# Performance work log

Hardware: AMD Instinct MI355X
Metric: run time of the kernel (lower is better)

The kernel has to match this reference:

```python
import math
import jax, jax.numpy as jnp
import numpy as np

B, N, DIM, E, G, TOPK, DEPTH = 64, 512, 128, 16, 32, 4, 1
HID = 4 * DIM
EPS = 1e-8
LAMBDA_INIT = 0.8 - 0.6 * math.exp(-0.3 * DEPTH)


def setup_inputs() -> dict:
    key = jax.random.key(0)
    ks = jax.random.split(key, 16)
    d = {}
    d["x"] = jax.random.normal(ks[0], (B, N, DIM), jnp.float32)
    d["bias"] = jnp.zeros((1,), jnp.float32)
    d["attn_scale"] = jnp.ones((DIM,), jnp.float32)
    d["ffn_scale"] = jnp.ones((DIM,), jnp.float32)
    d["Wr"] = jax.random.normal(ks[1], (DIM, E), jnp.float32) * 0.05
    d["br"] = jnp.zeros((E,), jnp.float32)
    d["E1"] = jax.random.uniform(ks[2], (2, E, N, G), jnp.float32)
    d["E2"] = jax.random.uniform(ks[3], (2, E, G, N), jnp.float32)
    d["lambda_q1"] = jax.random.normal(ks[4], (DIM,), jnp.float32) * 0.1
    d["lambda_k1"] = jax.random.normal(ks[5], (DIM,), jnp.float32) * 0.1
    d["lambda_q2"] = jax.random.normal(ks[6], (DIM,), jnp.float32) * 0.1
    d["lambda_k2"] = jax.random.normal(ks[7], (DIM,), jnp.float32) * 0.1
    d["outer_lambda"] = jnp.log(jnp.asarray(99.0, jnp.float32))
    d["W1"] = jax.random.normal(ks[8], (DIM, HID), jnp.float32) * 0.02
    d["b1"] = jnp.zeros((HID,), jnp.float32)
    d["W2"] = jax.random.normal(ks[9], (DIM, HID), jnp.float32) * 0.02
    d["b2"] = jnp.zeros((HID,), jnp.float32)
    d["W3"] = jax.random.normal(ks[10], (HID, DIM), jnp.float32) * 0.02
    d["b3"] = jnp.zeros((DIM,), jnp.float32)
    return d


def _rmsnorm(v, scale):
    # RMSNorm with p<0: full L2 norm over last dim, rms = ||v|| / sqrt(d)
    rms = jnp.linalg.norm(v, axis=-1, keepdims=True) * (DIM ** -0.5)
    return scale * (v / (rms + EPS))


def reference(x, bias, attn_scale, ffn_scale, Wr, br, E1, E2,
              lambda_q1, lambda_k1, lambda_q2, lambda_k2, outer_lambda,
              W1, b1, W2, b2, W3, b3):
    # ---- pre-norm ----
    xn = _rmsnorm(x, attn_scale)                       # [B,N,F]

    # ---- top-k routing (selector) ----
    route_logits = xn @ Wr + br                        # [B,N,E]
    gate = jax.nn.sigmoid(route_logits)
    _, topk_idx = jax.lax.top_k(gate + bias, TOPK)     # [B,N,K]
    mask = jnp.sum(jax.nn.one_hot(topk_idx, E, dtype=gate.dtype), axis=-2)  # [B,N,E]
    # sigmoid(route + log(mask)) == sigmoid(route) * mask (mask in {0,1})
    gated = gate * mask
    route = gated / jnp.sum(gated, axis=-1, keepdims=True)

    # ---- coefficient: concat([1], -(exp(q1.k1) - exp(q2.k2) + lambda_init)) ----
    l1 = jnp.exp(jnp.sum(lambda_q1 * lambda_k1))
    l2 = jnp.exp(jnp.sum(lambda_q2 * lambda_k2))
    lambda_full = -(l1 - l2 + LAMBDA_INIT)
    coef = jnp.concatenate([jnp.ones((1,), x.dtype), lambda_full[None]])  # [2]

    # ---- outer mixing matrix (convex comb of eye with itself -> eye, kept faithful) ----
    w = jax.nn.sigmoid(outer_lambda)
    eye = jnp.eye(DIM, dtype=x.dtype)
    outer = w * eye + (1.0 - w) * eye                  # [F,F]

    # ---- expert graph mixing: bik,e,ekid,ekdj,bjf,fc->bic ----
    A1 = jax.nn.softmax(E1, axis=-1)                   # [2,E,N,G]
    A2 = jax.nn.softmax(E2, axis=-1)                   # [2,E,G,N]
    M = jnp.einsum('ekid,ekdj->ekij', A1, A2)          # [2,E,N,N]
    s = jnp.einsum('bik,ekij->beij', route, M)         # [B,2,N,N]
    xc = jnp.einsum('bjf,fc->bjc', xn, outer)          # [B,N,F]
    attn = jnp.einsum('e,beij,bjc->bic', coef, s, xc)  # [B,N,F]

    x = x + attn

    # ---- SwiGLU FFN (dropout is identity at inference) ----
    xn2 = _rmsnorm(x, ffn_scale)
    h = jax.nn.silu(xn2 @ W1 + b1) * (xn2 @ W2 + b2)   # [B,N,4F]
    x = x + h @ W3 + b3
    return x, topk_idx
```

## Files before the change

### kernel.cpp

```cpp
#include <hip/hip_runtime.h>
#include <math.h>

#define B_ 64
#define N_ 512
#define DIM_ 128
#define E_ 16
#define G_ 32
#define TOPK_ 4
#define HID_ 512

constexpr int BN_ROWS = B_ * N_;

using bf16x8 = __attribute__((ext_vector_type(8))) short;
using s16x4  = __attribute__((ext_vector_type(4))) short;
using f32x4  = __attribute__((ext_vector_type(4))) float;

__device__ __forceinline__ float bf2f(short s) {
    union { unsigned u; float f; } x;
    x.u = ((unsigned)(unsigned short)s) << 16;
    return x.f;
}
__device__ __forceinline__ short f2bf(float f) {
    union { float f; unsigned u; } x;
    x.f = f;
    unsigned r = x.u + 0x7FFF + ((x.u >> 16) & 1);
    return (short)(r >> 16);
}

__device__ __forceinline__ bf16x8 frag_ld(const short* base, int row, int ks, int lhi) {
    int addr = row * 128 + (((ks * 64) + lhi * 16) ^ ((row & 7) << 4));
    return *(const bf16x8*)((const char*)base + addr);
}

constexpr int NPRE = BN_ROWS / 4;
constexpr int NXNT = B_ * 16;
constexpr int NSMG = 32 * 512 / 8;
constexpr int NSMN = 1024 / 4;
constexpr int NTW  = 64 * 3;
constexpr int NMISC = NPRE + NXNT + NSMG + NSMN + NTW + 1;

__global__ __launch_bounds__(256) void k_misc(
    const float* __restrict__ x, const float* __restrict__ attn_s,
    const float* __restrict__ Wr, const float* __restrict__ br, const float* __restrict__ bias,
    float* __restrict__ route, float* __restrict__ topk_out,
    short* __restrict__ xnT,
    const float* __restrict__ E1, short* __restrict__ A1nb,
    const float* __restrict__ E2, short* __restrict__ A2nb,
    const float* __restrict__ W1, const float* __restrict__ W2, const float* __restrict__ W3,
    short* __restrict__ W1T, short* __restrict__ W2T, short* __restrict__ W3T,
    const float* __restrict__ lq1, const float* __restrict__ lk1,
    const float* __restrict__ lq2, const float* __restrict__ lk2,
    float lam_init, float* __restrict__ lam_out) {
    __shared__ float xbuf[4][132];
    __shared__ float tb[32][129];
    __shared__ float invb[32];
    __shared__ float tw[32][33];
    int blk = blockIdx.x;
    int tid = threadIdx.x;

    if (blk < NPRE) {
        int w = tid >> 6, lane = tid & 63;
        int row = blk * 4 + w;
        float2 v = ((const float2*)(x + (size_t)row * DIM_))[lane];
        float ss = v.x * v.x + v.y * v.y;
        for (int off = 32; off; off >>= 1) ss += __shfl_xor(ss, off);
        float inv = 1.0f / (sqrtf(ss * (1.0f / DIM_)) + 1e-8f);
        float2 s = ((const float2*)attn_s)[lane];
        xbuf[w][lane * 2]     = v.x * inv * s.x;
        xbuf[w][lane * 2 + 1] = v.y * inv * s.y;
        int e = lane & 15, chunk = lane >> 4;
        float acc = 0.f;
#pragma unroll
        for (int j = 0; j < 32; ++j) {
            int d = chunk * 32 + j;
            acc += xbuf[w][d] * Wr[d * E_ + e];
        }
        acc += __shfl_xor(acc, 16);
        acc += __shfl_xor(acc, 32);
        float gate = 1.0f / (1.0f + expf(-(acc + br[e])));
        float vv = gate + bias[0];
        int rank = 0;
#pragma unroll
        for (int i = 0; i < 16; ++i) {
            float vi = __shfl(vv, i);
            rank += ((vi > vv) || (vi == vv && i < e)) ? 1 : 0;
        }
        bool selq = (rank < TOPK_) && (lane < 16);
        float contrib = selq ? gate : 0.f;
        float ssum = contrib;
        ssum += __shfl_xor(ssum, 1); ssum += __shfl_xor(ssum, 2);
        ssum += __shfl_xor(ssum, 4); ssum += __shfl_xor(ssum, 8);
        if (lane < 16) route[(size_t)row * E_ + e] = selq ? gate / ssum : 0.0f;
        if (selq) topk_out[(size_t)row * TOPK_ + rank] = (float)e;
        return;
    }
    blk -= NPRE;

    if (blk < NXNT) {
        int b = blk >> 4, j0 = (blk & 15) * 32;
        const float* src = x + (size_t)(b * 512 + j0) * 128;
        int r = tid >> 3, c8 = tid & 7;
#pragma unroll
        for (int it = 0; it < 4; ++it) {
            int c4 = c8 + it * 8;
            float4 w4 = *(const float4*)(src + (size_t)r * 128 + c4 * 4);
            tb[r][c4 * 4 + 0] = w4.x; tb[r][c4 * 4 + 1] = w4.y;
            tb[r][c4 * 4 + 2] = w4.z; tb[r][c4 * 4 + 3] = w4.w;
        }
        __syncthreads();
        int sg = tid & 7;
        float ps = 0.f;
#pragma unroll
        for (int j = 0; j < 16; ++j) { float e2 = tb[r][sg * 16 + j]; ps += e2 * e2; }
        ps += __shfl_xor(ps, 1); ps += __shfl_xor(ps, 2); ps += __shfl_xor(ps, 4);
        if (sg == 0) invb[r] = 1.0f / (sqrtf(ps * (1.0f / DIM_)) + 1e-8f);
        __syncthreads();
        int c = tid >> 1, half = tid & 1;
        float sc = attn_s[c];
        short ov[16];
#pragma unroll
        for (int j = 0; j < 16; ++j) {
            int jj = half * 16 + j;
            ov[j] = f2bf(tb[jj][c] * invb[jj] * sc);
        }
        short* dst = xnT + (size_t)(b * 128 + c) * 512 + j0 + half * 16;
        *(bf16x8*)dst = *(bf16x8*)ov;
        *(bf16x8*)(dst + 8) = *(bf16x8*)(ov + 8);
        return;
    }
    blk -= NXNT;

    if (blk < NSMG) {
        int row = blk * 8 + (tid >> 5);
        int l = tid & 31;
        float v = E1[(size_t)row * 32 + l];
        float m = v;
        for (int off = 16; off; off >>= 1) m = fmaxf(m, __shfl_xor(m, off));
        float ev = expf(v - m);
        float s = ev;
        for (int off = 16; off; off >>= 1) s += __shfl_xor(s, off);
        A1nb[(size_t)row * 32 + l] = f2bf(ev / s);
        return;
    }
    blk -= NSMG;

    if (blk < NSMN) {
        int row = blk * 4 + (tid >> 6);
        int l = tid & 63;
        const float* p = E2 + (size_t)row * 512;
        float v[8];
        float m = -1e30f;
#pragma unroll
        for (int j = 0; j < 8; ++j) { v[j] = p[l + j * 64]; m = fmaxf(m, v[j]); }
        for (int off = 32; off; off >>= 1) m = fmaxf(m, __shfl_xor(m, off));
        float s = 0.f;
#pragma unroll
        for (int j = 0; j < 8; ++j) { v[j] = expf(v[j] - m); s += v[j]; }
        for (int off = 32; off; off >>= 1) s += __shfl_xor(s, off);
        float inv = 1.0f / s;
        short* q = A2nb + (size_t)row * 512;
#pragma unroll
        for (int j = 0; j < 8; ++j) q[l + j * 64] = f2bf(v[j] * inv);
        return;
    }
    blk -= NSMN;

    if (blk < NTW) {
        int m = blk >> 6, tile = blk & 63;
        const float* S = (m == 0) ? W1 : (m == 1) ? W2 : W3;
        short* D = (m == 0) ? W1T : (m == 1) ? W2T : W3T;
        int R = (m == 2) ? 512 : 128, C = (m == 2) ? 128 : 512;
        int ctiles = C / 32;
        int r0 = (tile / ctiles) * 32, c0 = (tile % ctiles) * 32;
        int tx = tid & 31, ty = tid >> 5;
#pragma unroll
        for (int r = 0; r < 4; ++r) tw[ty * 4 + r][tx] = S[(size_t)(r0 + ty * 4 + r) * C + c0 + tx];
        __syncthreads();
#pragma unroll
        for (int r = 0; r < 4; ++r) D[(size_t)(c0 + ty * 4 + r) * R + r0 + tx] = f2bf(tw[tx][ty * 4 + r]);
        return;
    }

    if (tid < 64) {
        int l = tid;
        float s1 = lq1[l] * lk1[l] + lq1[l + 64] * lk1[l + 64];
        float s2 = lq2[l] * lk2[l] + lq2[l + 64] * lk2[l + 64];
        for (int off = 32; off; off >>= 1) {
            s1 += __shfl_xor(s1, off);
            s2 += __shfl_xor(s2, off);
        }
        if (l == 0) lam_out[0] = -(expf(s1) - expf(s2) + lam_init);
    }
}

__global__ __launch_bounds__(256) void k_gemm_y(const short* __restrict__ A2nb,
                                                const short* __restrict__ xnT,
                                                short* __restrict__ YT) {
    __shared__ short As[128 * 64];
    __shared__ short Bs[128 * 64];
    int id = blockIdx.x;
    int nid = ((id & 7) << 6) + (id >> 3);
    int m0 = (nid & 3) * 128;
    int be = nid >> 2, b = be >> 1, e = be & 1;
    int tid = threadIdx.x, lane = tid & 63, wid = tid >> 6;
    int l15 = lane & 15, lhi = lane >> 4;
    int wr = wid >> 1, wc = wid & 1;
    const short* Asrc = A2nb + (size_t)e * 512 * 512 + (size_t)m0 * 512;
    const short* Bsrc = xnT + (size_t)b * 128 * 512;
    bf16x8 av[4], bv[4];
#pragma unroll
    for (int r = 0; r < 4; ++r) {
        int idx = tid + r * 256, row = idx >> 3, slot = idx & 7;
        av[r] = *(const bf16x8*)(Asrc + (size_t)row * 512 + slot * 8);
        bv[r] = *(const bf16x8*)(Bsrc + (size_t)row * 512 + slot * 8);
    }
    f32x4 acc[4][4] = {};
    for (int step = 0; step < 8; ++step) {
        __syncthreads();
#pragma unroll
        for (int r = 0; r < 4; ++r) {
            int idx = tid + r * 256, row = idx >> 3, slot = idx & 7;
            *(bf16x8*)((char*)As + row * 128 + ((slot * 16) ^ ((row & 7) << 4))) = av[r];
            *(bf16x8*)((char*)Bs + row * 128 + ((slot * 16) ^ ((row & 7) << 4))) = bv[r];
        }
        __syncthreads();
        if (step < 7) {
            int k0 = (step + 1) * 64;
#pragma unroll
            for (int r = 0; r < 4; ++r) {
                int idx = tid + r * 256, row = idx >> 3, slot = idx & 7;
                av[r] = *(const bf16x8*)(Asrc + (size_t)row * 512 + k0 + slot * 8);
                bv[r] = *(const bf16x8*)(Bsrc + (size_t)row * 512 + k0 + slot * 8);
            }
        }
#pragma unroll
        for (int ks = 0; ks < 2; ++ks) {
            bf16x8 af[4], bfr[4];
#pragma unroll
            for (int i = 0; i < 4; ++i) af[i] = frag_ld(As, wr * 64 + i * 16 + l15, ks, lhi);
#pragma unroll
            for (int j = 0; j < 4; ++j) bfr[j] = frag_ld(Bs, wc * 64 + j * 16 + l15, ks, lhi);
#pragma unroll
            for (int i = 0; i < 4; ++i)
#pragma unroll
                for (int j = 0; j < 4; ++j)
                    acc[i][j] = __builtin_amdgcn_mfma_f32_16x16x32_bf16(af[i], bfr[j], acc[i][j], 0, 0, 0);
        }
    }
    short* Yb = YT + (size_t)b * 128 * 1024 + e * 512;
#pragma unroll
    for (int i = 0; i < 4; ++i) {
        int mbase = m0 + wr * 64 + i * 16 + lhi * 4;
#pragma unroll
        for (int j = 0; j < 4; ++j) {
            int n = wc * 64 + j * 16 + l15;
            s16x4 o;
#pragma unroll
            for (int q = 0; q < 4; ++q) o[q] = f2bf(acc[i][j][q]);
            *(s16x4*)(Yb + (size_t)n * 1024 + mbase) = o;
        }
    }
}

__global__ __launch_bounds__(256) void k_attn(const short* __restrict__ A1nb,
                                              const float* __restrict__ route,
                                              const short* __restrict__ YT,
                                              const float* __restrict__ x,
                                              const float* __restrict__ lam_p,
                                              const float* __restrict__ ffn_s,
                                              float* __restrict__ x1,
                                              short* __restrict__ xn2b) {
    __shared__ short As[64 * 64];
    __shared__ short Bs[128 * 64];
    __shared__ float ssbuf[2][64];
    int id = blockIdx.x;
    int nid = ((id & 7) << 6) + (id >> 3);
    int m0 = (nid & 7) * 64;
    int b = nid >> 3;
    float lam = lam_p[0];
    int tid = threadIdx.x, lane = tid & 63, wid = tid >> 6;
    int l15 = lane & 15, lhi = lane >> 4;
    int wr = wid >> 1, wc = wid & 1;
    float rv[2];
    bf16x8 araw[2], yv[4];
#pragma unroll
    for (int r = 0; r < 2; ++r) {
        int idx = tid + r * 256, row = idx >> 3, slot = idx & 7;
        int t = (slot >> 2);
        int gi = m0 + row;
        rv[r] = route[((size_t)b * 512 + gi) * 16 + (t & 15)];
        araw[r] = *(const bf16x8*)(A1nb + ((size_t)t * 512 + gi) * 32 + (slot & 3) * 8);
    }
#pragma unroll
    for (int r = 0; r < 4; ++r) {
        int idx = tid + r * 256, row = idx >> 3, slot = idx & 7;
        yv[r] = *(const bf16x8*)(YT + ((size_t)b * 128 + row) * 1024 + slot * 8);
    }
    f32x4 acc[2][4] = {};
    for (int step = 0; step < 16; ++step) {
        __syncthreads();
#pragma unroll
        for (int r = 0; r < 2; ++r) {
            int idx = tid + r * 256, row = idx >> 3, slot = idx & 7;
            bf16x8 o;
#pragma unroll
            for (int q = 0; q < 8; ++q) o[q] = f2bf(bf2f(araw[r][q]) * rv[r]);
            *(bf16x8*)((char*)As + row * 128 + ((slot * 16) ^ ((row & 7) << 4))) = o;
        }
#pragma unroll
        for (int r = 0; r < 4; ++r) {
            int idx = tid + r * 256, row = idx >> 3, slot = idx & 7;
            *(bf16x8*)((char*)Bs + row * 128 + ((slot * 16) ^ ((row & 7) << 4))) = yv[r];
        }
        __syncthreads();
        if (step < 15) {
            int sn = step + 1;
#pragma unroll
            for (int r = 0; r < 2; ++r) {
                int idx = tid + r * 256, row = idx >> 3, slot = idx & 7;
                int t = sn * 2 + (slot >> 2);
                int gi = m0 + row;
                rv[r] = route[((size_t)b * 512 + gi) * 16 + (t & 15)] * (t >= 16 ? lam : 1.0f);
                araw[r] = *(const bf16x8*)(A1nb + ((size_t)t * 512 + gi) * 32 + (slot & 3) * 8);
            }
#pragma unroll
            for (int r = 0; r < 4; ++r) {
                int idx = tid + r * 256, row = idx >> 3, slot = idx & 7;
                yv[r] = *(const bf16x8*)(YT + ((size_t)b * 128 + row) * 1024 + sn * 64 + slot * 8);
            }
        }
#pragma unroll
        for (int ks = 0; ks < 2; ++ks) {
            bf16x8 af[2], bfr[4];
#pragma unroll
            for (int i = 0; i < 2; ++i) af[i] = frag_ld(As, wr * 32 + i * 16 + l15, ks, lhi);
#pragma unroll
            for (int j = 0; j < 4; ++j) bfr[j] = frag_ld(Bs, wc * 64 + j * 16 + l15, ks, lhi);
#pragma unroll
            for (int i = 0; i < 2; ++i)
#pragma unroll
                for (int j = 0; j < 4; ++j)
                    acc[i][j] = __builtin_amdgcn_mfma_f32_16x16x32_bf16(af[i], bfr[j], acc[i][j], 0, 0, 0);
        }
    }
    float x1v[2][4][4];
    float pss[2][4] = {};
#pragma unroll
    for (int i = 0; i < 2; ++i) {
        int gibase = m0 + wr * 32 + i * 16 + lhi * 4;
#pragma unroll
        for (int j = 0; j < 4; ++j) {
            int n = wc * 64 + j * 16 + l15;
#pragma unroll
            for (int q = 0; q < 4; ++q) {
                size_t off = ((size_t)b * 512 + gibase + q) * 128 + n;
                float val = acc[i][j][q] + x[off];
                x1[off] = val;
                x1v[i][j][q] = val;
                pss[i][q] += val * val;
            }
        }
    }
#pragma unroll
    for (int i = 0; i < 2; ++i)
#pragma unroll
        for (int q = 0; q < 4; ++q) {
            float p = pss[i][q];
            p += __shfl_xor(p, 1); p += __shfl_xor(p, 2);
            p += __shfl_xor(p, 4); p += __shfl_xor(p, 8);
            pss[i][q] = p;
        }
    if (l15 == 0) {
#pragma unroll
        for (int i = 0; i < 2; ++i)
#pragma unroll
            for (int q = 0; q < 4; ++q)
                ssbuf[wc][wr * 32 + i * 16 + lhi * 4 + q] = pss[i][q];
    }
    __syncthreads();
#pragma unroll
    for (int i = 0; i < 2; ++i)
#pragma unroll
        for (int q = 0; q < 4; ++q) {
            int rowl = wr * 32 + i * 16 + lhi * 4 + q;
            float ssum = ssbuf[0][rowl] + ssbuf[1][rowl];
            float inv = 1.0f / (sqrtf(ssum * (1.0f / DIM_)) + 1e-8f);
#pragma unroll
            for (int j = 0; j < 4; ++j) {
                int n = wc * 64 + j * 16 + l15;
                xn2b[((size_t)b * 512 + m0 + rowl) * 128 + n] = f2bf(x1v[i][j][q] * inv * ffn_s[n]);
            }
        }
}

__global__ __launch_bounds__(256) void k_ffn1(const short* __restrict__ xn2b,
                                              const short* __restrict__ W1T, const float* __restrict__ b1,
                                              const short* __restrict__ W2T, const float* __restrict__ b2,
                                              short* __restrict__ h) {
    __shared__ short As[128 * 64];
    __shared__ short B1s[64 * 64];
    __shared__ short B2s[64 * 64];
    int id = blockIdx.x;
    int nid = ((id & 7) << 8) + (id >> 3);
    int n0 = (nid & 7) * 64;
    int m0 = (nid >> 3) * 128;
    int tid = threadIdx.x, lane = tid & 63, wid = tid >> 6;
    int l15 = lane & 15, lhi = lane >> 4;
    int wr = wid >> 1, wc = wid & 1;
    bf16x8 av[4], wv[4];
#pragma unroll
    for (int r = 0; r < 4; ++r) {
        int idx = tid + r * 256, row = idx >> 3, slot = idx & 7;
        av[r] = *(const bf16x8*)(xn2b + (size_t)(m0 + row) * 128 + slot * 8);
        int which = idx >> 9, brow = (idx >> 3) & 63;
        const short* S = which ? W2T : W1T;
        wv[r] = *(const bf16x8*)(S + (size_t)(n0 + brow) * 128 + slot * 8);
    }
    f32x4 acc1[4][2] = {}, acc2[4][2] = {};
    for (int step = 0; step < 2; ++step) {
        __syncthreads();
#pragma unroll
        for (int r = 0; r < 4; ++r) {
            int idx = tid + r * 256, row = idx >> 3, slot = idx & 7;
            *(bf16x8*)((char*)As + row * 128 + ((slot * 16) ^ ((row & 7) << 4))) = av[r];
            int which = idx >> 9, brow = (idx >> 3) & 63;
            short* D = which ? (short*)B2s : (short*)B1s;
            *(bf16x8*)((char*)D + brow * 128 + ((slot * 16) ^ ((brow & 7) << 4))) = wv[r];
        }
        __syncthreads();
        if (step == 0) {
#pragma unroll
            for (int r = 0; r < 4; ++r) {
                int idx = tid + r * 256, row = idx >> 3, slot = idx & 7;
                av[r] = *(const bf16x8*)(xn2b + (size_t)(m0 + row) * 128 + 64 + slot * 8);
                int which = idx >> 9, brow = (idx >> 3) & 63;
                const short* S = which ? W2T : W1T;
                wv[r] = *(const bf16x8*)(S + (size_t)(n0 + brow) * 128 + 64 + slot * 8);
            }
        }
#pragma unroll
        for (int ks = 0; ks < 2; ++ks) {
            bf16x8 af[4], b1f[2], b2f[2];
#pragma unroll
            for (int i = 0; i < 4; ++i) af[i] = frag_ld(As, wr * 64 + i * 16 + l15, ks, lhi);
#pragma unroll
            for (int j = 0; j < 2; ++j) {
                b1f[j] = frag_ld(B1s, wc * 32 + j * 16 + l15, ks, lhi);
                b2f[j] = frag_ld(B2s, wc * 32 + j * 16 + l15, ks, lhi);
            }
#pragma unroll
            for (int i = 0; i < 4; ++i)
#pragma unroll
                for (int j = 0; j < 2; ++j) {
                    acc1[i][j] = __builtin_amdgcn_mfma_f32_16x16x32_bf16(af[i], b1f[j], acc1[i][j], 0, 0, 0);
                    acc2[i][j] = __builtin_amdgcn_mfma_f32_16x16x32_bf16(af[i], b2f[j], acc2[i][j], 0, 0, 0);
                }
        }
    }
    __syncthreads();
#pragma unroll
    for (int i = 0; i < 4; ++i) {
        int mloc = wr * 64 + i * 16 + lhi * 4;
#pragma unroll
        for (int j = 0; j < 2; ++j) {
            int nloc = wc * 32 + j * 16 + l15;
            int n = n0 + nloc;
            float bb1 = b1[n], bb2 = b2[n];
#pragma unroll
            for (int q = 0; q < 4; ++q) {
                float a1 = acc1[i][j][q] + bb1;
                float a2 = acc2[i][j][q] + bb2;
                float hv = a1 / (1.0f + expf(-a1)) * a2;
                ((short*)As)[(mloc + q) * 64 + nloc] = f2bf(hv);
            }
        }
    }
    __syncthreads();
#pragma unroll
    for (int r = 0; r < 4; ++r) {
        int idx = tid + r * 256, row = idx >> 3, slot = idx & 7;
        *(bf16x8*)(h + (size_t)(m0 + row) * 512 + n0 + slot * 8) =
            *(const bf16x8*)((char*)As + row * 128 + slot * 16);
    }
}

__global__ __launch_bounds__(256) void k_ffn2(const short* __restrict__ h,
                                              const short* __restrict__ W3T, const float* __restrict__ b3,
                                              const float* __restrict__ x1,
                                              float* __restrict__ out) {
    __shared__ short As[64 * 64];
    __shared__ short Bs[128 * 64];
    int m0 = blockIdx.x * 64;
    int tid = threadIdx.x, lane = tid & 63, wid = tid >> 6;
    int l15 = lane & 15, lhi = lane >> 4;
    int wr = wid >> 1, wc = wid & 1;
    bf16x8 av[2], wv[4];
#pragma unroll
    for (int r = 0; r < 2; ++r) {
        int idx = tid + r * 256, row = idx >> 3, slot = idx & 7;
        av[r] = *(const bf16x8*)(h + (size_t)(m0 + row) * 512 + slot * 8);
    }
#pragma unroll
    for (int r = 0; r < 4; ++r) {
        int idx = tid + r * 256, row = idx >> 3, slot = idx & 7;
        wv[r] = *(const bf16x8*)(W3T + (size_t)row * 512 + slot * 8);
    }
    f32x4 acc[2][4] = {};
    for (int step = 0; step < 8; ++step) {
        __syncthreads();
#pragma unroll
        for (int r = 0; r < 2; ++r) {
            int idx = tid + r * 256, row = idx >> 3, slot = idx & 7;
            *(bf16x8*)((char*)As + row * 128 + ((slot * 16) ^ ((row & 7) << 4))) = av[r];
        }
#pragma unroll
        for (int r = 0; r < 4; ++r) {
            int idx = tid + r * 256, row = idx >> 3, slot = idx & 7;
            *(bf16x8*)((char*)Bs + row * 128 + ((slot * 16) ^ ((row & 7) << 4))) = wv[r];
        }
        __syncthreads();
        if (step < 7) {
            int k0 = (step + 1) * 64;
#pragma unroll
            for (int r = 0; r < 2; ++r) {
                int idx = tid + r * 256, row = idx >> 3, slot = idx & 7;
                av[r] = *(const bf16x8*)(h + (size_t)(m0 + row) * 512 + k0 + slot * 8);
            }
#pragma unroll
            for (int r = 0; r < 4; ++r) {
                int idx = tid + r * 256, row = idx >> 3, slot = idx & 7;
                wv[r] = *(const bf16x8*)(W3T + (size_t)row * 512 + k0 + slot * 8);
            }
        }
#pragma unroll
        for (int ks = 0; ks < 2; ++ks) {
            bf16x8 af[2], bfr[4];
#pragma unroll
            for (int i = 0; i < 2; ++i) af[i] = frag_ld(As, wr * 32 + i * 16 + l15, ks, lhi);
#pragma unroll
            for (int j = 0; j < 4; ++j) bfr[j] = frag_ld(Bs, wc * 64 + j * 16 + l15, ks, lhi);
#pragma unroll
            for (int i = 0; i < 2; ++i)
#pragma unroll
                for (int j = 0; j < 4; ++j)
                    acc[i][j] = __builtin_amdgcn_mfma_f32_16x16x32_bf16(af[i], bfr[j], acc[i][j], 0, 0, 0);
        }
    }
#pragma unroll
    for (int i = 0; i < 2; ++i) {
        int mbase = m0 + wr * 32 + i * 16 + lhi * 4;
#pragma unroll
        for (int j = 0; j < 4; ++j) {
            int n = wc * 64 + j * 16 + l15;
            float bv = b3[n];
#pragma unroll
            for (int q = 0; q < 4; ++q) {
                size_t off = (size_t)(mbase + q) * 128 + n;
                out[off] = acc[i][j][q] + x1[off] + bv;
            }
        }
    }
}

constexpr size_t ALIGN_UP(size_t x) { return (x + 255) & ~(size_t)255; }
constexpr size_t SZ_X1   = ALIGN_UP((size_t)BN_ROWS * DIM_ * 4);
constexpr size_t SZ_RT   = ALIGN_UP((size_t)BN_ROWS * E_ * 4);
constexpr size_t SZ_A1   = ALIGN_UP((size_t)32 * 512 * 32 * 2);
constexpr size_t SZ_A2   = ALIGN_UP((size_t)2 * 512 * 512 * 2);
constexpr size_t SZ_XNT  = ALIGN_UP((size_t)B_ * 128 * 512 * 2);
constexpr size_t SZ_YT   = ALIGN_UP((size_t)B_ * 128 * 1024 * 2);
constexpr size_t SZ_XN2B = ALIGN_UP((size_t)BN_ROWS * DIM_ * 2);
constexpr size_t SZ_H    = ALIGN_UP((size_t)BN_ROWS * HID_ * 2);
constexpr size_t SZ_WT   = ALIGN_UP((size_t)128 * 512 * 2);

extern "C" void kernel_launch(void* const* d_in, const int* in_sizes, int n_in,
                              void* d_out, int out_size, void* d_ws, size_t ws_size,
                              hipStream_t stream) {
    const float* x      = (const float*)d_in[0];
    const float* bias   = (const float*)d_in[1];
    const float* attn_s = (const float*)d_in[2];
    const float* ffn_s  = (const float*)d_in[3];
    const float* Wr     = (const float*)d_in[4];
    const float* br     = (const float*)d_in[5];
    const float* E1     = (const float*)d_in[6];
    const float* E2     = (const float*)d_in[7];
    const float* lq1    = (const float*)d_in[8];
    const float* lk1    = (const float*)d_in[9];
    const float* lq2    = (const float*)d_in[10];
    const float* lk2    = (const float*)d_in[11];
    const float* W1     = (const float*)d_in[13];
    const float* b1     = (const float*)d_in[14];
    const float* W2     = (const float*)d_in[15];
    const float* b2     = (const float*)d_in[16];
    const float* W3     = (const float*)d_in[17];
    const float* b3     = (const float*)d_in[18];

    char* p = (char*)d_ws;
    float* x1   = (float*)p;            p += SZ_X1;
    float* rt   = (float*)p;            p += SZ_RT;
    short* A1nb = (short*)p;            p += SZ_A1;
    short* A2nb = (short*)p;            p += SZ_A2;
    short* xnT  = (short*)p;            p += SZ_XNT;
    short* YT   = (short*)p;            p += SZ_YT;
    short* xn2b = (short*)p;            p += SZ_XN2B;
    short* h    = (short*)p;            p += SZ_H;
    short* W1T  = (short*)p;            p += SZ_WT;
    short* W2T  = (short*)p;            p += SZ_WT;
    short* W3T  = (short*)p;            p += SZ_WT;
    float* lam  = (float*)p;            p += 256;

    float* out_x   = (float*)d_out;
    float* out_idx = out_x + (size_t)BN_ROWS * DIM_;

    float lam_init = 0.8f - 0.6f * expf(-0.3f);

    hipLaunchKernelGGL(k_misc, dim3(NMISC), dim3(256), 0, stream,
                       x, attn_s, Wr, br, bias, rt, out_idx, xnT,
                       E1, A1nb, E2, A2nb, W1, W2, W3, W1T, W2T, W3T,
                       lq1, lk1, lq2, lk2, lam_init, lam);
    hipLaunchKernelGGL(k_gemm_y, dim3(512), dim3(256), 0, stream, A2nb, xnT, YT);
    hipLaunchKernelGGL(k_attn, dim3(512), dim3(256), 0, stream, A1nb, rt, YT, x, lam, ffn_s, x1, xn2b);
    hipLaunchKernelGGL(k_ffn1, dim3(2048), dim3(256), 0, stream, xn2b, W1T, b1, W2T, b2, h);
    hipLaunchKernelGGL(k_ffn2, dim3(512), dim3(256), 0, stream, h, W3T, b3, x1, out_x);
}
```

Baseline: 199.5 us.

## Double-buffer GEMM tiles with direct global-to-LDS loads across kernels

Replaces the register-staged global→LDS copies in the four GEMM kernels with buffer_load-to-LDS (global_load_lds) into double-buffered shared tiles. The swizzle is applied on the source address instead. One barrier per k-step replaces two, and the next tile's loads overlap the current MFMA work. k_attn interleaves a register path for the route-scaled A tile with an async path for the B tile. The router in k_misc also drops its shared buffer in favour of wave shuffles. LDS use doubles, which may lower occupancy, and the hand-placed waitcnt/barrier ordering must stay correct.

Result: slower. 203.7 us (+2.1%).

```diff
diff --git a/kernel.cpp b/kernel.cpp
--- a/kernel.cpp
+++ b/kernel.cpp
@@ -30,6 +30,24 @@
 __device__ __forceinline__ bf16x8 frag_ld(const short* base, int row, int ks, int lhi) {
     int addr = row * 128 + (((ks * 64) + lhi * 16) ^ ((row & 7) << 4));
     return *(const bf16x8*)((const char*)base + addr);
+}
+
+typedef __attribute__((address_space(3))) void lds_vt;
+typedef __attribute__((address_space(1))) const void gbl_vt;
+__device__ __forceinline__ void gl2lds(const void* g, void* l) {
+    __builtin_amdgcn_global_load_lds((gbl_vt*)g, (lds_vt*)l, 16, 0, 0);
+}
+__device__ __forceinline__ void vm0_bar() {
+    asm volatile("s_waitcnt vmcnt(0)" ::: "memory");
+    __builtin_amdgcn_sched_barrier(0);
+    __builtin_amdgcn_s_barrier();
+    __builtin_amdgcn_sched_barrier(0);
+}
+__device__ __forceinline__ void lgkm0_bar() {
+    asm volatile("s_waitcnt lgkmcnt(0)" ::: "memory");
+    __builtin_amdgcn_sched_barrier(0);
+    __builtin_amdgcn_s_barrier();
+    __builtin_amdgcn_sched_barrier(0);
 }
 
 constexpr int NPRE = BN_ROWS / 4;
@@ -51,7 +69,6 @@
     const float* __restrict__ lq1, const float* __restrict__ lk1,
     const float* __restrict__ lq2, const float* __restrict__ lk2,
     float lam_init, float* __restrict__ lam_out) {
-    __shared__ float xbuf[4][132];
     __shared__ float tb[32][129];
     __shared__ float invb[32];
     __shared__ float tw[32][33];
@@ -66,14 +83,17 @@
         for (int off = 32; off; off >>= 1) ss += __shfl_xor(ss, off);
         float inv = 1.0f / (sqrtf(ss * (1.0f / DIM_)) + 1e-8f);
         float2 s = ((const float2*)attn_s)[lane];
-        xbuf[w][lane * 2]     = v.x * inv * s.x;
-        xbuf[w][lane * 2 + 1] = v.y * inv * s.y;
+        float xn0 = v.x * inv * s.x;
+        float xn1 = v.y * inv * s.y;
         int e = lane & 15, chunk = lane >> 4;
         float acc = 0.f;
 #pragma unroll
-        for (int j = 0; j < 32; ++j) {
-            int d = chunk * 32 + j;
-            acc += xbuf[w][d] * Wr[d * E_ + e];
+        for (int j = 0; j < 16; ++j) {
+            int srcl = chunk * 16 + j;
+            float a0 = __shfl(xn0, srcl);
+            float a1 = __shfl(xn1, srcl);
+            int d0 = chunk * 32 + 2 * j;
+            acc += a0 * Wr[d0 * E_ + e] + a1 * Wr[(d0 + 1) * E_ + e];
         }
         acc += __shfl_xor(acc, 16);
         acc += __shfl_xor(acc, 32);
@@ -196,8 +216,10 @@
 __global__ __launch_bounds__(256) void k_gemm_y(const short* __restrict__ A2nb,
                                                 const short* __restrict__ xnT,
                                                 short* __restrict__ YT) {
-    __shared__ short As[128 * 64];
-    __shared__ short Bs[128 * 64];
+    alignas(16) __shared__ short As0[128 * 64];
+    alignas(16) __shared__ short Bs0[128 * 64];
+    alignas(16) __shared__ short As1[128 * 64];
+    alignas(16) __shared__ short Bs1[128 * 64];
     int id = blockIdx.x;
     int nid = ((id & 7) << 6) + (id >> 3);
     int m0 = (nid & 3) * 128;
@@ -207,39 +229,32 @@
     int wr = wid >> 1, wc = wid & 1;
     const short* Asrc = A2nb + (size_t)e * 512 * 512 + (size_t)m0 * 512;
     const short* Bsrc = xnT + (size_t)b * 128 * 512;
-    bf16x8 av[4], bv[4];
-#pragma unroll
-    for (int r = 0; r < 4; ++r) {
-        int idx = tid + r * 256, row = idx >> 3, slot = idx & 7;
-        av[r] = *(const bf16x8*)(Asrc + (size_t)row * 512 + slot * 8);
-        bv[r] = *(const bf16x8*)(Bsrc + (size_t)row * 512 + slot * 8);
-    }
+    int row8 = lane >> 3;
+    int chunk8 = (lane & 7) ^ row8;
+
+    auto stage = [&](short* Ad, short* Bd, int k0) {
+#pragma unroll
+        for (int t = 0; t < 4; ++t) {
+            int i = wid * 4 + t;
+            int row = i * 8 + row8;
+            gl2lds(Asrc + (size_t)row * 512 + k0 + chunk8 * 8, (char*)Ad + i * 1024);
+            gl2lds(Bsrc + (size_t)row * 512 + k0 + chunk8 * 8, (char*)Bd + i * 1024);
+        }
+    };
     f32x4 acc[4][4] = {};
-    for (int step = 0; step < 8; ++step) {
-        __syncthreads();
-#pragma unroll
-        for (int r = 0; r < 4; ++r) {
-            int idx = tid + r * 256, row = idx >> 3, slot = idx & 7;
-            *(bf16x8*)((char*)As + row * 128 + ((slot * 16) ^ ((row & 7) << 4))) = av[r];
-            *(bf16x8*)((char*)Bs + row * 128 + ((slot * 16) ^ ((row & 7) << 4))) = bv[r];
-        }
-        __syncthreads();
-        if (step < 7) {
-            int k0 = (step + 1) * 64;
-#pragma unroll
-            for (int r = 0; r < 4; ++r) {
-                int idx = tid + r * 256, row = idx >> 3, slot = idx & 7;
-                av[r] = *(const bf16x8*)(Asrc + (size_t)row * 512 + k0 + slot * 8);
-                bv[r] = *(const bf16x8*)(Bsrc + (size_t)row * 512 + k0 + slot * 8);
-            }
-        }
+    stage(As0, Bs0, 0);
+    for (int s = 0; s < 8; ++s) {
+        vm0_bar();
+        const short* Ac = (s & 1) ? As1 : As0;
+        const short* Bc = (s & 1) ? Bs1 : Bs0;
+        if (s < 7) stage((s & 1) ? As0 : As1, (s & 1) ? Bs0 : Bs1, (s + 1) * 64);
 #pragma unroll
         for (int ks = 0; ks < 2; ++ks) {
             bf16x8 af[4], bfr[4];
 #pragma unroll
-            for (int i = 0; i < 4; ++i) af[i] = frag_ld(As, wr * 64 + i * 16 + l15, ks, lhi);
-#pragma unroll
-            for (int j = 0; j < 4; ++j) bfr[j] = frag_ld(Bs, wc * 64 + j * 16 + l15, ks, lhi);
+            for (int i = 0; i < 4; ++i) af[i] = frag_ld(Ac, wr * 64 + i * 16 + l15, ks, lhi);
+#pragma unroll
+            for (int j = 0; j < 4; ++j) bfr[j] = frag_ld(Bc, wc * 64 + j * 16 + l15, ks, lhi);
 #pragma unroll
             for (int i = 0; i < 4; ++i)
 #pragma unroll
@@ -270,8 +285,10 @@
                                               const float* __restrict__ ffn_s,
                                               float* __restrict__ x1,
                                               short* __restrict__ xn2b) {
-    __shared__ short As[64 * 64];
-    __shared__ short Bs[128 * 64];
+    alignas(16) __shared__ short Ab0[64 * 64];
+    alignas(16) __shared__ short Ab1[64 * 64];
+    alignas(16) __shared__ short Bb0[128 * 64];
+    alignas(16) __shared__ short Bb1[128 * 64];
     __shared__ float ssbuf[2][64];
     int id = blockIdx.x;
     int nid = ((id & 7) << 6) + (id >> 3);
@@ -281,67 +298,75 @@
     int tid = threadIdx.x, lane = tid & 63, wid = tid >> 6;
     int l15 = lane & 15, lhi = lane >> 4;
     int wr = wid >> 1, wc = wid & 1;
-    float rv[2];
-    bf16x8 araw[2], yv[4];
-#pragma unroll
-    for (int r = 0; r < 2; ++r) {
-        int idx = tid + r * 256, row = idx >> 3, slot = idx & 7;
-        int t = (slot >> 2);
-        int gi = m0 + row;
-        rv[r] = route[((size_t)b * 512 + gi) * 16 + (t & 15)];
-        araw[r] = *(const bf16x8*)(A1nb + ((size_t)t * 512 + gi) * 32 + (slot & 3) * 8);
-    }
-#pragma unroll
-    for (int r = 0; r < 4; ++r) {
-        int idx = tid + r * 256, row = idx >> 3, slot = idx & 7;
-        yv[r] = *(const bf16x8*)(YT + ((size_t)b * 128 + row) * 1024 + slot * 8);
-    }
+    const short* YTb = YT + (size_t)b * 128 * 1024;
+    int row8 = lane >> 3;
+    int chunk8 = (lane & 7) ^ row8;
+
+    auto stageB = [&](short* Bd, int k0) {
+#pragma unroll
+        for (int t = 0; t < 4; ++t) {
+            int i = wid * 4 + t;
+            int row = i * 8 + row8;
+            gl2lds(YTb + (size_t)row * 1024 + k0 + chunk8 * 8, (char*)Bd + i * 1024);
+        }
+    };
+    auto loadA = [&](float (&rv)[2], bf16x8 (&ar)[2], int sn) {
+#pragma unroll
+        for (int r = 0; r < 2; ++r) {
+            int idx = tid + r * 256, rowl = idx >> 3, slot = idx & 7;
+            int t = sn * 2 + (slot >> 2);
+            int gi = m0 + rowl;
+            rv[r] = route[((size_t)b * 512 + gi) * 16 + (t & 15)] * (t >= 16 ? lam : 1.0f);
+            ar[r] = *(const bf16x8*)(A1nb + ((size_t)t * 512 + gi) * 32 + (slot & 3) * 8);
+        }
+    };
+    auto writeA = [&](short* dst, float (&rv)[2], bf16x8 (&ar)[2]) {
+#pragma unroll
+        for (int r = 0; r < 2; ++r) {
+            int idx = tid + r * 256, rowl = idx >> 3, slot = idx & 7;
+            bf16x8 o;
+#pragma unroll
+            for (int q = 0; q < 8; ++q) o[q] = f2bf(bf2f(ar[r][q]) * rv[r]);
+            *(bf16x8*)((char*)dst + rowl * 128 + ((slot * 16) ^ ((rowl & 7) << 4))) = o;
+        }
+    };
     f32x4 acc[2][4] = {};
-    for (int step = 0; step < 16; ++step) {
-        __syncthreads();
-#pragma unroll
-        for (int r = 0; r < 2; ++r) {
-            int idx = tid + r * 256, row = idx >> 3, slot = idx & 7;
-            bf16x8 o;
-#pragma unroll
-            for (int q = 0; q < 8; ++q) o[q] = f2bf(bf2f(araw[r][q]) * rv[r]);
-            *(bf16x8*)((char*)As + row * 128 + ((slot * 16) ^ ((row & 7) << 4))) = o;
-        }
-#pragma unroll
-        for (int r = 0; r < 4; ++r) {
-            int idx = tid + r * 256, row = idx >> 3, slot = idx & 7;
-            *(bf16x8*)((char*)Bs + row * 128 + ((slot * 16) ^ ((row & 7) << 4))) = yv[r];
-        }
-        __syncthreads();
-        if (step < 15) {
-            int sn = step + 1;
-#pragma unroll
-            for (int r = 0; r < 2; ++r) {
-                int idx = tid + r * 256, row = idx >> 3, slot = idx & 7;
-                int t = sn * 2 + (slot >> 2);
-                int gi = m0 + row;
-                rv[r] = route[((size_t)b * 512 + gi) * 16 + (t & 15)] * (t >= 16 ? lam : 1.0f);
-                araw[r] = *(const bf16x8*)(A1nb + ((size_t)t * 512 + gi) * 32 + (slot & 3) * 8);
-            }
-#pragma unroll
-            for (int r = 0; r < 4; ++r) {
-                int idx = tid + r * 256, row = idx >> 3, slot = idx & 7;
-                yv[r] = *(const bf16x8*)(YT + ((size_t)b * 128 + row) * 1024 + sn * 64 + slot * 8);
-            }
-        }
+    auto compute = [&](const short* Ac, const short* Bc) {
 #pragma unroll
         for (int ks = 0; ks < 2; ++ks) {
             bf16x8 af[2], bfr[4];
 #pragma unroll
-            for (int i = 0; i < 2; ++i) af[i] = frag_ld(As, wr * 32 + i * 16 + l15, ks, lhi);
-#pragma unroll
-            for (int j = 0; j < 4; ++j) bfr[j] = frag_ld(Bs, wc * 64 + j * 16 + l15, ks, lhi);
+            for (int i = 0; i < 2; ++i) af[i] = frag_ld(Ac, wr * 32 + i * 16 + l15, ks, lhi);
+#pragma unroll
+            for (int j = 0; j < 4; ++j) bfr[j] = frag_ld(Bc, wc * 64 + j * 16 + l15, ks, lhi);
 #pragma unroll
             for (int i = 0; i < 2; ++i)
 #pragma unroll
                 for (int j = 0; j < 4; ++j)
                     acc[i][j] = __builtin_amdgcn_mfma_f32_16x16x32_bf16(af[i], bfr[j], acc[i][j], 0, 0, 0);
         }
+    };
+
+    float rv0[2], rv1[2];
+    bf16x8 ar0[2], ar1[2];
+    stageB(Bb0, 0);
+    loadA(rv0, ar0, 0);
+    for (int sp = 0; sp < 8; ++sp) {
+        int s = sp * 2;
+        vm0_bar();
+        stageB(Bb1, (s + 1) * 64);
+        loadA(rv1, ar1, s + 1);
+        writeA(Ab0, rv0, ar0);
+        lgkm0_bar();
+        compute(Ab0, Bb0);
+        vm0_bar();
+        if (s + 2 < 16) {
+            stageB(Bb0, (s + 2) * 64);
+            loadA(rv0, ar0, s + 2);
+        }
+        writeA(Ab1, rv1, ar1);
+        lgkm0_bar();
+        compute(Ab1, Bb1);
     }
     float x1v[2][4][4];
     float pss[2][4] = {};
@@ -397,9 +422,12 @@
                                               const short* __restrict__ W1T, const float* __restrict__ b1,
                                               const short* __restrict__ W2T, const float* __restrict__ b2,
                                               short* __restrict__ h) {
-    __shared__ short As[128 * 64];
-    __shared__ short B1s[64 * 64];
-    __shared__ short B2s[64 * 64];
+    alignas(16) __shared__ short As0[128 * 64];
+    alignas(16) __shared__ short B10[64 * 64];
+    alignas(16) __shared__ short B20[64 * 64];
+    alignas(16) __shared__ short As1[128 * 64];
+    alignas(16) __shared__ short B11[64 * 64];
+    alignas(16) __shared__ short B21[64 * 64];
     int id = blockIdx.x;
     int nid = ((id & 7) << 8) + (id >> 3);
     int n0 = (nid & 7) * 64;
@@ -407,46 +435,42 @@
     int tid = threadIdx.x, lane = tid & 63, wid = tid >> 6;
     int l15 = lane & 15, lhi = lane >> 4;
     int wr = wid >> 1, wc = wid & 1;
-    bf16x8 av[4], wv[4];
-#pragma unroll
-    for (int r = 0; r < 4; ++r) {
-        int idx = tid + r * 256, row = idx >> 3, slot = idx & 7;
-        av[r] = *(const bf16x8*)(xn2b + (size_t)(m0 + row) * 128 + slot * 8);
-        int which = idx >> 9, brow = (idx >> 3) & 63;
-        const short* S = which ? W2T : W1T;
-        wv[r] = *(const bf16x8*)(S + (size_t)(n0 + brow) * 128 + slot * 8);
-    }
+    int row8 = lane >> 3;
+    int chunk8 = (lane & 7) ^ row8;
+
+    auto stage = [&](short* Ad, short* B1d, short* B2d, int k0) {
+#pragma unroll
+        for (int t = 0; t < 8; ++t) {
+            int i = wid * 8 + t;
+            if (i < 16) {
+                int row = i * 8 + row8;
+                gl2lds(xn2b + (size_t)(m0 + row) * 128 + k0 + chunk8 * 8, (char*)Ad + i * 1024);
+            } else if (i < 24) {
+                int ii = i - 16, row = ii * 8 + row8;
+                gl2lds(W1T + (size_t)(n0 + row) * 128 + k0 + chunk8 * 8, (char*)B1d + ii * 1024);
+            } else {
+                int ii = i - 24, row = ii * 8 + row8;
+                gl2lds(W2T + (size_t)(n0 + row) * 128 + k0 + chunk8 * 8, (char*)B2d + ii * 1024);
+            }
+        }
+    };
     f32x4 acc1[4][2] = {}, acc2[4][2] = {};
-    for (int step = 0; step < 2; ++step) {
-        __syncthreads();
-#pragma unroll
-        for (int r = 0; r < 4; ++r) {
-            int idx = tid + r * 256, row = idx >> 3, slot = idx & 7;
-            *(bf16x8*)((char*)As + row * 128 + ((slot * 16) ^ ((row & 7) << 4))) = av[r];
-            int which = idx >> 9, brow = (idx >> 3) & 63;
-            short* D = which ? (short*)B2s : (short*)B1s;
-            *(bf16x8*)((char*)D + brow * 128 + ((slot * 16) ^ ((brow & 7) << 4))) = wv[r];
-        }
-        __syncthreads();
-        if (step == 0) {
-#pragma unroll
-            for (int r = 0; r < 4; ++r) {
-                int idx = tid + r * 256, row = idx >> 3, slot = idx & 7;
-                av[r] = *(const bf16x8*)(xn2b + (size_t)(m0 + row) * 128 + 64 + slot * 8);
-                int which = idx >> 9, brow = (idx >> 3) & 63;
-                const short* S = which ? W2T : W1T;
-                wv[r] = *(const bf16x8*)(S + (size_t)(n0 + brow) * 128 + 64 + slot * 8);
-            }
-        }
+    stage(As0, B10, B20, 0);
+    for (int s = 0; s < 2; ++s) {
+        vm0_bar();
+        const short* Ac = s ? As1 : As0;
+        const short* B1c = s ? B11 : B10;
+        const short* B2c = s ? B21 : B20;
+        if (s == 0) stage(As1, B11, B21, 64);
 #pragma unroll
         for (int ks = 0; ks < 2; ++ks) {
             bf16x8 af[4], b1f[2], b2f[2];
 #pragma unroll
-            for (int i = 0; i < 4; ++i) af[i] = frag_ld(As, wr * 64 + i * 16 + l15, ks, lhi);
+            for (int i = 0; i < 4; ++i) af[i] = frag_ld(Ac, wr * 64 + i * 16 + l15, ks, lhi);
 #pragma unroll
             for (int j = 0; j < 2; ++j) {
-                b1f[j] = frag_ld(B1s, wc * 32 + j * 16 + l15, ks, lhi);
-                b2f[j] = frag_ld(B2s, wc * 32 + j * 16 + l15, ks, lhi);
+                b1f[j] = frag_ld(B1c, wc * 32 + j * 16 + l15, ks, lhi);
+                b2f[j] = frag_ld(B2c, wc * 32 + j * 16 + l15, ks, lhi);
             }
 #pragma unroll
             for (int i = 0; i < 4; ++i)
@@ -471,16 +495,17 @@
                 float a1 = acc1[i][j][q] + bb1;
                 float a2 = acc2[i][j][q] + bb2;
                 float hv = a1 / (1.0f + expf(-a1)) * a2;
-                ((short*)As)[(mloc + q) * 64 + nloc] = f2bf(hv);
+                ((short*)As0)[(mloc + q) * 64 + nloc] = f2bf(hv);
             }
         }
     }
     __syncthreads();
 #pragma unroll
     for (int r = 0; r < 4; ++r) {
-        int idx = tid + r * 256, row = idx >> 3, slot = idx & 7;
+        int idx = tid + r * 256;
+        int row = idx >> 3, slot = idx & 7;
         *(bf16x8*)(h + (size_t)(m0 + row) * 512 + n0 + slot * 8) =
-            *(const bf16x8*)((char*)As + row * 128 + slot * 16);
+            *(const bf16x8*)((char*)As0 + row * 128 + slot * 16);
     }
 }
 
@@ -488,57 +513,44 @@
                                               const short* __restrict__ W3T, const float* __restrict__ b3,
                                               const float* __restrict__ x1,
                                               float* __restrict__ out) {
-    __shared__ short As[64 * 64];
-    __shared__ short Bs[128 * 64];
+    alignas(16) __shared__ short As0[64 * 64];
+    alignas(16) __shared__ short Bs0[128 * 64];
+    alignas(16) __shared__ short As1[64 * 64];
+    alignas(16) __shared__ short Bs1[128 * 64];
     int m0 = blockIdx.x * 64;
     int tid = threadIdx.x, lane = tid & 63, wid = tid >> 6;
     int l15 = lane & 15, lhi = lane >> 4;
     int wr = wid >> 1, wc = wid & 1;
-    bf16x8 av[2], wv[4];
-#pragma unroll
-    for (int r = 0; r < 2; ++r) {
-        int idx = tid + r * 256, row = idx >> 3, slot = idx & 7;
-        av[r] = *(const bf16x8*)(h + (size_t)(m0 + row) * 512 + slot * 8);
-    }
-#pragma unroll
-    for (int r = 0; r < 4; ++r) {
-        int idx = tid + r * 256, row = idx >> 3, slot = idx & 7;
-        wv[r] = *(const bf16x8*)(W3T + (size_t)row * 512 + slot * 8);
-    }
+    int row8 = lane >> 3;
+    int chunk8 = (lane & 7) ^ row8;
+
+    auto stage = [&](short* Ad, short* Bd, int k0) {
+#pragma unroll
+        for (int t = 0; t < 6; ++t) {
+            int i = wid * 6 + t;
+            if (i < 8) {
+                int row = i * 8 + row8;
+                gl2lds(h + (size_t)(m0 + row) * 512 + k0 + chunk8 * 8, (char*)Ad + i * 1024);
+            } else {
+                int ii = i - 8, row = ii * 8 + row8;
+                gl2lds(W3T + (size_t)row * 512 + k0 + chunk8 * 8, (char*)Bd + ii * 1024);
+            }
+        }
+    };
     f32x4 acc[2][4] = {};
-    for (int step = 0; step < 8; ++step) {
-        __syncthreads();
-#pragma unroll
-        for (int r = 0; r < 2; ++r) {
-            int idx = tid + r * 256, row = idx >> 3, slot = idx & 7;
-            *(bf16x8*)((char*)As + row * 128 + ((slot * 16) ^ ((row & 7) << 4))) = av[r];
-        }
-#pragma unroll
-        for (int r = 0; r < 4; ++r) {
-            int idx = tid + r * 256, row = idx >> 3, slot = idx & 7;
-            *(bf16x8*)((char*)Bs + row * 128 + ((slot * 16) ^ ((row & 7) << 4))) = wv[r];
-        }
-        __syncthreads();
-        if (step < 7) {
-            int k0 = (step + 1) * 64;
-#pragma unroll
-            for (int r = 0; r < 2; ++r) {
-                int idx = tid + r * 256, row = idx >> 3, slot = idx & 7;
-                av[r] = *(const bf16x8*)(h + (size_t)(m0 + row) * 512 + k0 + slot * 8);
-            }
-#pragma unroll
-            for (int r = 0; r < 4; ++r) {
-                int idx = tid + r * 256, row = idx >> 3, slot = idx & 7;
-                wv[r] = *(const bf16x8*)(W3T + (size_t)row * 512 + k0 + slot * 8);
-            }
-        }
+    stage(As0, Bs0, 0);
+    for (int s = 0; s < 8; ++s) {
+        vm0_bar();
+        const short* Ac = (s & 1) ? As1 : As0;
+        const short* Bc = (s & 1) ? Bs1 : Bs0;
+        if (s < 7) stage((s & 1) ? As0 : As1, (s & 1) ? Bs0 : Bs1, (s + 1) * 64);
 #pragma unroll
         for (int ks = 0; ks < 2; ++ks) {
             bf16x8 af[2], bfr[4];
 #pragma unroll
-            for (int i = 0; i < 2; ++i) af[i] = frag_ld(As, wr * 32 + i * 16 + l15, ks, lhi);
-#pragma unroll
-            for (int j = 0; j < 4; ++j) bfr[j] = frag_ld(Bs, wc * 64 + j * 16 + l15, ks, lhi);
+            for (int i = 0; i < 2; ++i) af[i] = frag_ld(Ac, wr * 32 + i * 16 + l15, ks, lhi);
+#pragma unroll
+            for (int j = 0; j < 4; ++j) bfr[j] = frag_ld(Bc, wc * 64 + j * 16 + l15, ks, lhi);
 #pragma unroll
             for (int i = 0; i < 2; ++i)
 #pragma unroll
```
